# Kernel tuning notes

Measured on AMD Instinct MI355X. Metric: run time of the kernel, lower is better.

## Reference

```python
import jax, jax.numpy as jnp
import numpy as np

VOCAB, EMB, HID, OUT = 32000, 512, 1024, 512
B, S = 64, 256


def setup_inputs() -> dict:
    key = jax.random.key(0)
    ks = jax.random.split(key, 16)
    def xavier(k, shape):
        bound = np.sqrt(6.0 / (shape[0] + shape[1]))
        return jax.random.uniform(k, shape, jnp.float32, -bound, bound)
    return {
        "tokens": jax.random.randint(ks[0], (B, S), 0, VOCAB),
        "emb": jax.random.normal(ks[1], (VOCAB, EMB), jnp.float32) * 0.02,
        "W_xi": xavier(ks[2], (EMB, HID)),
        "W_xf": xavier(ks[3], (EMB, HID)),
        "W_xo": xavier(ks[4], (EMB, HID)),
        "W_xc": xavier(ks[5], (EMB, HID)),
        "W_hi": xavier(ks[6], (HID, HID)),
        "W_hf": xavier(ks[7], (HID, HID)),
        "W_ho": xavier(ks[8], (HID, HID)),
        "W_hc": xavier(ks[9], (HID, HID)),
        "W_hy": xavier(ks[10], (HID, OUT)),
        "b_i": jnp.zeros((HID,), jnp.float32),
        "b_f": jnp.zeros((HID,), jnp.float32),
        "b_o": jnp.zeros((HID,), jnp.float32),
        "b_c": jnp.zeros((HID,), jnp.float32),
        "b_hy": jnp.zeros((OUT,), jnp.float32),
    }


def reference(tokens, emb, W_xi, W_xf, W_xo, W_xc, W_hi, W_hf, W_ho, W_hc,
              W_hy, b_i, b_f, b_o, b_c, b_hy):
    # Embedding lookup for all timesteps (dropout is identity at inference).
    x = emb[tokens]  # [B, S, E]
    # Precompute input-to-gate projections in one batched GEMM per gate.
    gx_i = jnp.einsum('bse,eh->bsh', x, W_xi) + b_i
    gx_f = jnp.einsum('bse,eh->bsh', x, W_xf) + b_f
    gx_o = jnp.einsum('bse,eh->bsh', x, W_xo) + b_o
    gx_c = jnp.einsum('bse,eh->bsh', x, W_xc) + b_c
    # Time-major stacked gates: [S, B, 4, H]
    g = jnp.stack([gx_i, gx_f, gx_o, gx_c], axis=2).transpose(1, 0, 2, 3)

    h0 = jnp.zeros((tokens.shape[0], W_hi.shape[0]), x.dtype)
    c0 = jnp.zeros_like(h0)

    def step(carry, g_t):
        h, c = carry
        i = jax.nn.sigmoid(g_t[:, 0] + h @ W_hi)
        f = jax.nn.sigmoid(g_t[:, 1] + h @ W_hf)
        o = jax.nn.sigmoid(g_t[:, 2] + h @ W_ho)
        cc = jnp.tanh(g_t[:, 3] + h @ W_hc)
        c = f * c + i * cc
        h = o * jnp.tanh(c)
        return (h, c), None

    (h, c), _ = jax.lax.scan(step, (h0, c0), g)
    return h @ W_hy + b_hy  # [B, OUT]
```

## Files before the change

### kernel.cpp

```cpp
#include <hip/hip_runtime.h>
#include <hip/hip_bf16.h>

#define EMBN   512
#define HIDN   1024
#define OUTN   512
#define BBN    64
#define SSN    256
#define NBLK   256
#define PSTR   20

typedef __attribute__((ext_vector_type(8))) short bf16x8;
typedef __attribute__((ext_vector_type(4))) float f32x4;
typedef __attribute__((ext_vector_type(4))) int int4v;
typedef unsigned short us;
typedef unsigned long long ull;

static __device__ __forceinline__ us f2bf(float x) {
  unsigned int u = __float_as_uint(x);
  unsigned int r = (u + 0x7fffu + ((u >> 16) & 1u)) >> 16;
  return (us)r;
}
static __device__ __forceinline__ float bf2f(us u) {
  unsigned int v = ((unsigned int)u) << 16;
  return __uint_as_float(v);
}

__global__ void pack_w(const float* __restrict__ wxi, const float* __restrict__ wxf,
                       const float* __restrict__ wxo, const float* __restrict__ wxc,
                       const float* __restrict__ whi, const float* __restrict__ whf,
                       const float* __restrict__ who, const float* __restrict__ whc,
                       us* __restrict__ Whip, us* __restrict__ Wlop) {
  int idx = blockIdx.x * 256 + threadIdx.x;
  int lane = idx & 63;
  int kt   = (idx >> 6) % 48;
  int j    = idx / (48 * 64);
  int q = lane & 15, g = q >> 2, r = q & 3;
  int hd = 4 * j + r;
  int kb = kt * 32 + ((lane >> 4) << 3);
  const float* wx = (g == 0) ? wxi : (g == 1) ? wxf : (g == 2) ? wxo : wxc;
  const float* wh = (g == 0) ? whi : (g == 1) ? whf : (g == 2) ? who : whc;
  long obase = (long)idx * 8;
  #pragma unroll
  for (int jj = 0; jj < 8; ++jj) {
    int k = kb + jj;
    float v = (k < EMBN) ? wx[(long)k * HIDN + hd] : wh[(long)(k - EMBN) * HIDN + hd];
    us hi = f2bf(v);
    us lo = f2bf(v - bf2f(hi));
    Whip[obase + jj] = hi;
    Wlop[obase + jj] = lo;
  }
}

__global__ void pack_x(const int* __restrict__ tokens, const float* __restrict__ emb,
                       us* __restrict__ Xhi, us* __restrict__ Xlo) {
  int idx = blockIdx.x * 256 + threadIdx.x;
  int k = idx & 511;
  int b = (idx >> 9) & 63;
  int t = idx >> 15;
  int tok = tokens[b * SSN + t];
  float v = emb[(long)tok * EMBN + k];
  us hi = f2bf(v);
  Xhi[idx] = hi;
  Xlo[idx] = f2bf(v - bf2f(hi));
}

#define XISS(A, c) { _Pragma("unroll") for (int q = 0; q < 4; ++q) { \
      A[2*q]   = *(const bf16x8*)(xh + (((c)*4 + q) << 5)); \
      A[2*q+1] = *(const bf16x8*)(xl + (((c)*4 + q) << 5)); } }
#define XCON(A, c) { _Pragma("unroll") for (int q = 0; q < 4; ++q) { \
      const int kt = (c)*4 + q; \
      bf16x8 w0 = *(const bf16x8*)(WHi + (kt << 9) + (lane << 3)); \
      bf16x8 w1 = *(const bf16x8*)(WLo + (kt << 9) + (lane << 3)); \
      accA = __builtin_amdgcn_mfma_f32_16x16x32_bf16(w0, A[2*q],   accA, 0, 0, 0); \
      accB = __builtin_amdgcn_mfma_f32_16x16x32_bf16(w0, A[2*q+1], accB, 0, 0, 0); \
      accC = __builtin_amdgcn_mfma_f32_16x16x32_bf16(w1, A[2*q],   accC, 0, 0, 0); } }
#define HISS(A, c) { _Pragma("unroll") for (int q = 0; q < 4; ++q) { \
      A[2*q]   = *(const bf16x8*)(hh + (((c)*4 + q) << 5)); \
      A[2*q+1] = *(const bf16x8*)(hl + (((c)*4 + q) << 5)); } }
#define HCON(A, c) { _Pragma("unroll") for (int q = 0; q < 4; ++q) { \
      const int kt = 16 + (c)*4 + q; \
      bf16x8 w0 = *(const bf16x8*)(WHi + (kt << 9) + (lane << 3)); \
      bf16x8 w1 = *(const bf16x8*)(WLo + (kt << 9) + (lane << 3)); \
      accA = __builtin_amdgcn_mfma_f32_16x16x32_bf16(w0, A[2*q],   accA, 0, 0, 0); \
      accB = __builtin_amdgcn_mfma_f32_16x16x32_bf16(w0, A[2*q+1], accB, 0, 0, 0); \
      accC = __builtin_amdgcn_mfma_f32_16x16x32_bf16(w1, A[2*q],   accC, 0, 0, 0); } }

__launch_bounds__(256, 1)
__global__ void lstm_persist(const us* __restrict__ Whip, const us* __restrict__ Wlop,
                             const us* __restrict__ Xhi, const us* __restrict__ Xlo,
                             us* Hhi, us* Hlo, float* hfin, int* flags,
                             const float* __restrict__ biP, const float* __restrict__ bfP,
                             const float* __restrict__ boP, const float* __restrict__ bcP,
                             int K) {
  extern __shared__ char smem[];
  us* WHi = (us*)smem;
  us* WLo = WHi + 24576;
  float* preact = (float*)(smem + 98304);

  const int j = blockIdx.x, tid = threadIdx.x;
  const int wv = tid >> 6, lane = tid & 63;
  const int Km = K - 1;
  const bool ROT = (K != 256);

  {
    const uint4* shi = (const uint4*)(Whip + (long)j * 24576);
    const uint4* slo = (const uint4*)(Wlop + (long)j * 24576);
    uint4* dhi = (uint4*)WHi;
    uint4* dlo = (uint4*)WLo;
    for (int i = tid; i < 3072; i += 256) { dhi[i] = shi[i]; dlo[i] = slo[i]; }
  }
  const int gb = tid >> 2, gr = tid & 3;
  const float bi_r = biP[4 * j + gr], bf_r = bfP[4 * j + gr];
  const float bo_r = boP[4 * j + gr], bc_r = bcP[4 * j + gr];
  float c_reg = 0.f;

  const int mrow = (wv << 4) + (lane & 15);
  const int kj = (lane >> 4) << 3;
  const int p0 = (lane >> 4) << 2;
  __syncthreads();

  #pragma unroll 1
  for (int t = 0; t < SSN; ++t) {
    f32x4 accA = {0.f, 0.f, 0.f, 0.f};
    f32x4 accB = {0.f, 0.f, 0.f, 0.f};
    f32x4 accC = {0.f, 0.f, 0.f, 0.f};

    {
      const us* xh = Xhi + ((long)t << 15) + (mrow << 9) + kj;
      const us* xl = Xlo + ((long)t << 15) + (mrow << 9) + kj;
      bf16x8 XA[8], XB[8];
      XISS(XA, 0) XISS(XB, 1)
      __builtin_amdgcn_sched_barrier(0);
      XCON(XA, 0) XISS(XA, 2)
      __builtin_amdgcn_sched_barrier(0);
      XCON(XB, 1) XISS(XB, 3)
      __builtin_amdgcn_sched_barrier(0);
      XCON(XA, 2) XCON(XB, 3)
    }

    if (t > 0) {
      if (wv == 0) {
        const int* fp = flags + (lane << 2);
        int4v f;
        do {
          asm volatile("global_load_dwordx4 %0, %1, off sc0 sc1\n\t"
                       "s_waitcnt vmcnt(0)"
                       : "=&v"(f) : "v"(fp) : "memory");
        } while (__any((f.x < t) | (f.y < t) | (f.z < t) | (f.w < t)));
      }
      __syncthreads();
      if (ROT && (t & Km) == 0)
        __builtin_amdgcn_fence(__ATOMIC_ACQUIRE, "agent");

      const int cur = t & Km;
      const us* hh = Hhi + (((long)cur * BBN + mrow) << 10) + kj;
      const us* hl = Hlo + (((long)cur * BBN + mrow) << 10) + kj;
      bf16x8 HA[8], HB[8], HC[8], HD[8];
      HISS(HA, 0) HISS(HB, 1) HISS(HC, 2) HISS(HD, 3)
      __builtin_amdgcn_sched_barrier(0);
      HCON(HA, 0) HISS(HA, 4)
      __builtin_amdgcn_sched_barrier(0);
      HCON(HB, 1) HISS(HB, 5)
      __builtin_amdgcn_sched_barrier(0);
      HCON(HC, 2) HISS(HC, 6)
      __builtin_amdgcn_sched_barrier(0);
      HCON(HD, 3) HISS(HD, 7)
      __builtin_amdgcn_sched_barrier(0);
      HCON(HA, 4) HCON(HB, 5) HCON(HC, 6) HCON(HD, 7)
    }

    {
      f32x4 acc = accA + accB;
      acc = acc + accC;
      *(f32x4*)(preact + mrow * PSTR + p0) = acc;
    }
    __syncthreads();

    {
      float pi = preact[gb * PSTR + gr]      + bi_r;
      float pf = preact[gb * PSTR + 4 + gr]  + bf_r;
      float po = preact[gb * PSTR + 8 + gr]  + bo_r;
      float pc = preact[gb * PSTR + 12 + gr] + bc_r;
      float vi = 1.f / (1.f + expf(-pi));
      float vf = 1.f / (1.f + expf(-pf));
      float vo = 1.f / (1.f + expf(-po));
      float vc = tanhf(pc);
      c_reg = vf * c_reg + vi * vc;
      float h = vo * tanhf(c_reg);
      if (t == SSN - 1) hfin[(gb << 10) + 4 * j + gr] = h;
      us hh_ = f2bf(h);
      us hl_ = f2bf(h - bf2f(hh_));

      unsigned int hpair = (unsigned int)hh_ | ((unsigned int)hl_ << 16);
      const int base = lane & ~3;
      unsigned int g0 = (unsigned int)__shfl((int)hpair, base);
      unsigned int g1 = (unsigned int)__shfl((int)hpair, base + 1);
      unsigned int g2 = (unsigned int)__shfl((int)hpair, base + 2);
      unsigned int g3 = (unsigned int)__shfl((int)hpair, base + 3);
      unsigned int hi01 = (g0 & 0xffffu) | (g1 << 16);
      unsigned int hi23 = (g2 & 0xffffu) | (g3 << 16);
      unsigned int lo01 = (g0 >> 16)     | (g1 & 0xffff0000u);
      unsigned int lo23 = (g2 >> 16)     | (g3 & 0xffff0000u);
      ull hiq = ((ull)hi23 << 32) | (ull)hi01;
      ull loq = ((ull)lo23 << 32) | (ull)lo01;

      const long nxt = (t + 1) & Km;
      if (gr == 0) {
        __hip_atomic_store((ull*)(Hhi + ((nxt * BBN + gb) << 10) + 4 * j), hiq,
                           __ATOMIC_RELAXED, __HIP_MEMORY_SCOPE_AGENT);
        __hip_atomic_store((ull*)(Hlo + ((nxt * BBN + gb) << 10) + 4 * j), loq,
                           __ATOMIC_RELAXED, __HIP_MEMORY_SCOPE_AGENT);
      }
      asm volatile("s_waitcnt vmcnt(0)" ::: "memory");
      __syncthreads();
      if (tid == 0)
        __hip_atomic_store(&flags[j], t + 1, __ATOMIC_RELAXED, __HIP_MEMORY_SCOPE_AGENT);
    }
  }
}

__global__ void out_gemm(const float* __restrict__ hfin, const float* __restrict__ Why,
                         const float* __restrict__ bhy, float* __restrict__ out) {
  int b = blockIdx.x, n = threadIdx.x;
  const float* h = hfin + (b << 10);
  float acc = 0.f;
  #pragma unroll 8
  for (int k = 0; k < HIDN; ++k) acc = fmaf(h[k], Why[(k << 9) + n], acc);
  out[(b << 9) + n] = acc + bhy[n];
}

extern "C" void kernel_launch(void* const* d_in, const int* in_sizes, int n_in,
                              void* d_out, int out_size, void* d_ws, size_t ws_size,
                              hipStream_t stream) {
  const int*   tokens = (const int*)d_in[0];
  const float* emb    = (const float*)d_in[1];
  const float* Wxi    = (const float*)d_in[2];
  const float* Wxf    = (const float*)d_in[3];
  const float* Wxo    = (const float*)d_in[4];
  const float* Wxc    = (const float*)d_in[5];
  const float* Whi_   = (const float*)d_in[6];
  const float* Whf    = (const float*)d_in[7];
  const float* Who    = (const float*)d_in[8];
  const float* Whc    = (const float*)d_in[9];
  const float* Why    = (const float*)d_in[10];
  const float* bi     = (const float*)d_in[11];
  const float* bfv    = (const float*)d_in[12];
  const float* bo     = (const float*)d_in[13];
  const float* bc     = (const float*)d_in[14];
  const float* bhy    = (const float*)d_in[15];
  float* outp = (float*)d_out;

  char* ws = (char*)d_ws;
  size_t off = 0;
  auto carve = [&](size_t bytes) -> void* {
    void* p = ws + off;
    off += (bytes + 255) & ~(size_t)255;
    return p;
  };
  us*    Whip = (us*)carve(12582912);
  us*    Wlop = (us*)carve(12582912);
  us*    Xhi  = (us*)carve(16777216);
  us*    Xlo  = (us*)carve(16777216);
  float* hfin = (float*)carve(262144);
  int*   flags = (int*)carve(1024);

  size_t rem = (ws_size > off) ? (ws_size - off) : 0;
  int K = 256;
  while (K > 4 && (size_t)2 * (size_t)K * 131072 + 512 > rem) K >>= 1;
  if ((size_t)2 * (size_t)K * 131072 + 512 > rem) {
    (void)hipMemsetAsync(d_out, 0, (size_t)out_size * 4, stream);
    return;
  }
  us* Hhi = (us*)carve((size_t)K * 131072);
  us* Hlo = (us*)carve((size_t)K * 131072);

  (void)hipMemsetAsync(flags, 0, 1024, stream);

  pack_w<<<3072, 256, 0, stream>>>(Wxi, Wxf, Wxo, Wxc, Whi_, Whf, Who, Whc, Whip, Wlop);
  pack_x<<<32768, 256, 0, stream>>>(tokens, emb, Xhi, Xlo);

  (void)hipFuncSetAttribute((const void*)lstm_persist,
                            hipFuncAttributeMaxDynamicSharedMemorySize, 103424);
  lstm_persist<<<NBLK, 256, 103424, stream>>>(Whip, Wlop, Xhi, Xlo, Hhi, Hlo,
                                              hfin, flags, bi, bfv, bo, bc, K);
  out_gemm<<<BBN, OUTN, 0, stream>>>(hfin, Why, bhy, outp);
}
```

Measured before the change: 3.150 ms.

## Use per-wave flags for LSTM step sync and overlap next-step input GEMM

Each wave handles a fixed set of batch rows, so the block-wide flag and the block barriers become per-wave flags. A wave now waits only on the matching wave in every other block. The input-projection MFMAs for step t+1 are issued right after h for step t is published, so they run while the wave waits for the other blocks instead of sitting on the critical path. The spin loop adds s_sleep to cut polling pressure. In exchange there are four times as many flags to poll, and correctness relies on each wave reading only the preact rows it wrote.

```diff
diff --git a/kernel.cpp b/kernel.cpp
--- a/kernel.cpp
+++ b/kernel.cpp
@@ -117,40 +117,43 @@
   const int mrow = (wv << 4) + (lane & 15);
   const int kj = (lane >> 4) << 3;
   const int p0 = (lane >> 4) << 2;
+  int* const flagsP = flags + (wv << 8);
   __syncthreads();
+
+  f32x4 accA = {0.f, 0.f, 0.f, 0.f};
+  f32x4 accB = {0.f, 0.f, 0.f, 0.f};
+  f32x4 accC = {0.f, 0.f, 0.f, 0.f};
+
+  {
+    const us* xh = Xhi + (mrow << 9) + kj;
+    const us* xl = Xlo + (mrow << 9) + kj;
+    bf16x8 XA[8], XB[8];
+    XISS(XA, 0) XISS(XB, 1)
+    __builtin_amdgcn_sched_barrier(0);
+    XCON(XA, 0) XISS(XA, 2)
+    __builtin_amdgcn_sched_barrier(0);
+    XCON(XB, 1) XISS(XB, 3)
+    __builtin_amdgcn_sched_barrier(0);
+    XCON(XA, 2) XCON(XB, 3)
+  }
 
   #pragma unroll 1
   for (int t = 0; t < SSN; ++t) {
-    f32x4 accA = {0.f, 0.f, 0.f, 0.f};
-    f32x4 accB = {0.f, 0.f, 0.f, 0.f};
-    f32x4 accC = {0.f, 0.f, 0.f, 0.f};
-
-    {
-      const us* xh = Xhi + ((long)t << 15) + (mrow << 9) + kj;
-      const us* xl = Xlo + ((long)t << 15) + (mrow << 9) + kj;
-      bf16x8 XA[8], XB[8];
-      XISS(XA, 0) XISS(XB, 1)
-      __builtin_amdgcn_sched_barrier(0);
-      XCON(XA, 0) XISS(XA, 2)
-      __builtin_amdgcn_sched_barrier(0);
-      XCON(XB, 1) XISS(XB, 3)
-      __builtin_amdgcn_sched_barrier(0);
-      XCON(XA, 2) XCON(XB, 3)
-    }
-
     if (t > 0) {
-      if (wv == 0) {
-        const int* fp = flags + (lane << 2);
+      if (ROT && (t & Km) == 0)
+        __builtin_amdgcn_fence(__ATOMIC_ACQUIRE, "agent");
+
+      {
+        const int* fp = flagsP + (lane << 2);
         int4v f;
-        do {
+        for (;;) {
           asm volatile("global_load_dwordx4 %0, %1, off sc0 sc1\n\t"
                        "s_waitcnt vmcnt(0)"
                        : "=&v"(f) : "v"(fp) : "memory");
-        } while (__any((f.x < t) | (f.y < t) | (f.z < t) | (f.w < t)));
+          if (!__any((f.x < t) | (f.y < t) | (f.z < t) | (f.w < t))) break;
+          __builtin_amdgcn_s_sleep(2);
+        }
       }
-      __syncthreads();
-      if (ROT && (t & Km) == 0)
-        __builtin_amdgcn_fence(__ATOMIC_ACQUIRE, "agent");
 
       const int cur = t & Km;
       const us* hh = Hhi + (((long)cur * BBN + mrow) << 10) + kj;
@@ -174,7 +177,6 @@
       acc = acc + accC;
       *(f32x4*)(preact + mrow * PSTR + p0) = acc;
     }
-    __syncthreads();
 
     {
       float pi = preact[gb * PSTR + gr]      + bi_r;
@@ -187,34 +189,51 @@
       float vc = tanhf(pc);
       c_reg = vf * c_reg + vi * vc;
       float h = vo * tanhf(c_reg);
-      if (t == SSN - 1) hfin[(gb << 10) + 4 * j + gr] = h;
-      us hh_ = f2bf(h);
-      us hl_ = f2bf(h - bf2f(hh_));
-
-      unsigned int hpair = (unsigned int)hh_ | ((unsigned int)hl_ << 16);
-      const int base = lane & ~3;
-      unsigned int g0 = (unsigned int)__shfl((int)hpair, base);
-      unsigned int g1 = (unsigned int)__shfl((int)hpair, base + 1);
-      unsigned int g2 = (unsigned int)__shfl((int)hpair, base + 2);
-      unsigned int g3 = (unsigned int)__shfl((int)hpair, base + 3);
-      unsigned int hi01 = (g0 & 0xffffu) | (g1 << 16);
-      unsigned int hi23 = (g2 & 0xffffu) | (g3 << 16);
-      unsigned int lo01 = (g0 >> 16)     | (g1 & 0xffff0000u);
-      unsigned int lo23 = (g2 >> 16)     | (g3 & 0xffff0000u);
-      ull hiq = ((ull)hi23 << 32) | (ull)hi01;
-      ull loq = ((ull)lo23 << 32) | (ull)lo01;
-
-      const long nxt = (t + 1) & Km;
-      if (gr == 0) {
-        __hip_atomic_store((ull*)(Hhi + ((nxt * BBN + gb) << 10) + 4 * j), hiq,
-                           __ATOMIC_RELAXED, __HIP_MEMORY_SCOPE_AGENT);
-        __hip_atomic_store((ull*)(Hlo + ((nxt * BBN + gb) << 10) + 4 * j), loq,
-                           __ATOMIC_RELAXED, __HIP_MEMORY_SCOPE_AGENT);
+
+      if (t == SSN - 1) {
+        hfin[(gb << 10) + 4 * j + gr] = h;
+      } else {
+        us hh_ = f2bf(h);
+        us hl_ = f2bf(h - bf2f(hh_));
+        unsigned int hpair = (unsigned int)hh_ | ((unsigned int)hl_ << 16);
+        const int base = lane & ~3;
+        unsigned int g0 = (unsigned int)__shfl((int)hpair, base);
+        unsigned int g1 = (unsigned int)__shfl((int)hpair, base + 1);
+        unsigned int g2 = (unsigned int)__shfl((int)hpair, base + 2);
+        unsigned int g3 = (unsigned int)__shfl((int)hpair, base + 3);
+        unsigned int hi01 = (g0 & 0xffffu) | (g1 << 16);
+        unsigned int hi23 = (g2 & 0xffffu) | (g3 << 16);
+        unsigned int lo01 = (g0 >> 16)     | (g1 & 0xffff0000u);
+        unsigned int lo23 = (g2 >> 16)     | (g3 & 0xffff0000u);
+        ull hiq = ((ull)hi23 << 32) | (ull)hi01;
+        ull loq = ((ull)lo23 << 32) | (ull)lo01;
+
+        const long nxt = (long)((t + 1) & Km);
+        if (gr == 0) {
+          __hip_atomic_store((ull*)(Hhi + ((nxt * BBN + gb) << 10) + 4 * j), hiq,
+                             __ATOMIC_RELAXED, __HIP_MEMORY_SCOPE_AGENT);
+          __hip_atomic_store((ull*)(Hlo + ((nxt * BBN + gb) << 10) + 4 * j), loq,
+                             __ATOMIC_RELAXED, __HIP_MEMORY_SCOPE_AGENT);
+        }
+
+        const us* xh = Xhi + ((long)(t + 1) << 15) + (mrow << 9) + kj;
+        const us* xl = Xlo + ((long)(t + 1) << 15) + (mrow << 9) + kj;
+        bf16x8 XA[8], XB[8];
+        XISS(XA, 0) XISS(XB, 1)
+        asm volatile("s_waitcnt vmcnt(0)" ::: "memory");
+        if (lane == 0)
+          __hip_atomic_store(&flagsP[j], t + 1,
+                             __ATOMIC_RELAXED, __HIP_MEMORY_SCOPE_AGENT);
+        __builtin_amdgcn_sched_barrier(0);
+        accA = {0.f, 0.f, 0.f, 0.f};
+        accB = {0.f, 0.f, 0.f, 0.f};
+        accC = {0.f, 0.f, 0.f, 0.f};
+        XCON(XA, 0) XISS(XA, 2)
+        __builtin_amdgcn_sched_barrier(0);
+        XCON(XB, 1) XISS(XB, 3)
+        __builtin_amdgcn_sched_barrier(0);
+        XCON(XA, 2) XCON(XB, 3)
       }
-      asm volatile("s_waitcnt vmcnt(0)" ::: "memory");
-      __syncthreads();
-      if (tid == 0)
-        __hip_atomic_store(&flags[j], t + 1, __ATOMIC_RELAXED, __HIP_MEMORY_SCOPE_AGENT);
     }
   }
 }
@@ -262,11 +281,11 @@
   us*    Xhi  = (us*)carve(16777216);
   us*    Xlo  = (us*)carve(16777216);
   float* hfin = (float*)carve(262144);
-  int*   flags = (int*)carve(1024);
+  int*   flags = (int*)carve(4096);
 
   size_t rem = (ws_size > off) ? (ws_size - off) : 0;
   int K = 256;
-  while (K > 4 && (size_t)2 * (size_t)K * 131072 + 512 > rem) K >>= 1;
+  while (K > 8 && (size_t)2 * (size_t)K * 131072 + 512 > rem) K >>= 1;
   if ((size_t)2 * (size_t)K * 131072 + 512 > rem) {
     (void)hipMemsetAsync(d_out, 0, (size_t)out_size * 4, stream);
     return;
@@ -274,7 +293,7 @@
   us* Hhi = (us*)carve((size_t)K * 131072);
   us* Hlo = (us*)carve((size_t)K * 131072);
 
-  (void)hipMemsetAsync(flags, 0, 1024, stream);
+  (void)hipMemsetAsync(flags, 0, 4096, stream);
 
   pack_w<<<3072, 256, 0, stream>>>(Wxi, Wxf, Wxo, Wxc, Whi_, Whf, Who, Whc, Whip, Wlop);
   pack_x<<<32768, 256, 0, stream>>>(tokens, emb, Xhi, Xlo);
```

After: 2.821 ms. -10.4%, faster.
